# Kernel tuning notes

Hardware: AMD Instinct MI355X
Metric: run time of the kernel (lower is better)

Reference implementation:

```python
import jax, jax.numpy as jnp
import numpy as np

N = 50000
E = 1600000
NFEAT = 128
NHID = 128
NEG_SLOPE_ATT = 0.2   # GATConv attention leaky_relu
NEG_SLOPE_ACT = 0.01  # F.leaky_relu default between layers


def setup_inputs() -> dict:
    key = jax.random.key(0)
    ks = jax.random.split(key, 12)
    x = jax.random.normal(ks[0], (N, NFEAT), dtype=jnp.float32)
    edge_index = jax.random.randint(ks[1], (2, E), 0, N, dtype=jnp.int64)
    s1 = 1.0 / np.sqrt(NFEAT)
    s2 = 1.0 / np.sqrt(NHID)
    return {
        "x": x,
        "edge_index": edge_index,
        "W1": jax.random.normal(ks[2], (NFEAT, NHID), dtype=jnp.float32) * s1,
        "att_src1": jax.random.normal(ks[3], (NHID,), dtype=jnp.float32) * s2,
        "att_dst1": jax.random.normal(ks[4], (NHID,), dtype=jnp.float32) * s2,
        "b1": jnp.zeros((NHID,), dtype=jnp.float32),
        "W2": jax.random.normal(ks[5], (NHID, NHID), dtype=jnp.float32) * s2,
        "att_src2": jax.random.normal(ks[6], (NHID,), dtype=jnp.float32) * s2,
        "att_dst2": jax.random.normal(ks[7], (NHID,), dtype=jnp.float32) * s2,
        "b2": jnp.zeros((NHID,), dtype=jnp.float32),
    }


def _gat_conv(x, src, dst, W, a_src, a_dst, b):
    # single-head GATConv (PyG defaults), self-loops already in src/dst
    h = x @ W                                  # [N, nhid]
    alpha_s = h @ a_src                        # [N]
    alpha_d = h @ a_dst                        # [N]
    e = jax.nn.leaky_relu(alpha_s[src] + alpha_d[dst], NEG_SLOPE_ATT)  # [E']
    # softmax over incoming edges per destination node
    m = jax.ops.segment_max(e, dst, num_segments=N)
    e = jnp.exp(e - m[dst])
    denom = jax.ops.segment_sum(e, dst, num_segments=N)
    alpha = e / (denom[dst] + 1e-16)
    out = jax.ops.segment_sum(h[src] * alpha[:, None], dst, num_segments=N)
    return out + b


def reference(x, edge_index, W1, att_src1, att_dst1, b1, W2, att_src2, att_dst2, b2):
    loops = jnp.arange(N, dtype=edge_index.dtype)
    src = jnp.concatenate([edge_index[0], loops])  # add_self_loops=True
    dst = jnp.concatenate([edge_index[1], loops])
    h = _gat_conv(x, src, dst, W1, att_src1, att_dst1, b1)
    h = jax.nn.leaky_relu(h, NEG_SLOPE_ACT)
    out = _gat_conv(h, src, dst, W2, att_src2, att_dst2, b2)
    return out
```

## Files before the change

### kernel.cpp

```cpp
#include <hip/hip_runtime.h>
#include <hip/hip_fp16.h>

constexpr int N  = 50000;
constexpr int E  = 1600000;
constexpr int ET = E + N;
constexpr int NF = 128;
constexpr int BSH = 128;
constexpr int NB = (N + BSH - 1) / BSH;
constexpr int CAP = 8192;
constexpr int EPB  = 8192;
constexpr int NBLK = (ET + EPB - 1) / EPB;
constexpr int PACKW_BLKS = (2 * NF * NF + 1023) / 1024;
constexpr int GEMM1_BLKS = (N + 127) / 128;
constexpr int SCAPW = 128;

typedef _Float16 half8 __attribute__((ext_vector_type(8)));
typedef float    f32x4 __attribute__((ext_vector_type(4)));

__global__ __launch_bounds__(1024) void k_scatter_packw(
    const int* __restrict__ ei, int* __restrict__ bcur, int* __restrict__ packed,
    const float* __restrict__ W1, const float* __restrict__ W2,
    __half* __restrict__ P1, __half* __restrict__ P2) {
    int t = threadIdx.x;
    if (blockIdx.x >= NBLK) {
        int tid = (blockIdx.x - NBLK) * 1024 + t;
        if (tid >= 2 * NF * NF) return;
        int which = tid >> 14;
        int id = tid & (NF * NF - 1);
        int k = id >> 7, n = id & 127;
        const float* W = which ? W2 : W1;
        __half* P = which ? P2 : P1;
        int ks = k >> 5, r = k & 31, ct = n >> 4;
        int lane = ((r >> 3) << 4) | (n & 15);
        int j = r & 7;
        P[((ks * 8 + ct) * 64 + lane) * 8 + j] = __float2half_rn(W[k * NF + n]);
        return;
    }
    __shared__ int h[NB], lcur[NB], garr[NB];
    for (int i = t; i < NB; i += 1024) h[i] = 0;
    __syncthreads();
    int base = blockIdx.x * EPB;
    int pk[EPB / 1024];
    int bk[EPB / 1024];
#pragma unroll
    for (int k = 0; k < EPB / 1024; ++k) {
        int i = base + k * 1024 + t;
        if (i < ET) {
            int s, d;
            if (i < E) { s = ei[i]; d = ei[E + i]; } else { s = i - E; d = i - E; }
            bk[k] = d >> 7;
            pk[k] = s | ((d & (BSH - 1)) << 16);
            atomicAdd(&h[bk[k]], 1);
        } else bk[k] = -1;
    }
    __syncthreads();
    for (int i = t; i < NB; i += 1024) {
        lcur[i] = 0;
        garr[i] = i * CAP + (h[i] ? atomicAdd(&bcur[i], h[i]) : 0);
    }
    __syncthreads();
#pragma unroll
    for (int k = 0; k < EPB / 1024; ++k) {
        if (bk[k] >= 0) {
            int p = garr[bk[k]] + atomicAdd(&lcur[bk[k]], 1);
            packed[p] = pk[k];
        }
    }
}

template <typename AT>
__device__ __forceinline__ void gemm_rows16(
    const AT* __restrict__ A, const half8* __restrict__ BP,
    const float* __restrict__ asv, const float* __restrict__ adv,
    __half* __restrict__ H16, float* __restrict__ AS, float* __restrict__ AD,
    int base, int lane) {
    int row_a = base + (lane & 15);
    if (row_a >= N) row_a = N - 1;
    const AT* Arow = A + (size_t)row_a * NF;

    f32x4 acc[8] = {};
#pragma unroll
    for (int ks = 0; ks < 4; ++ks) {
        int eo = (ks * 4 + (lane >> 4)) * 8;
        half8 a;
        if constexpr (sizeof(AT) == 4) {
            float4 u = *(const float4*)(Arow + eo);
            float4 v = *(const float4*)(Arow + eo + 4);
            a[0] = (_Float16)u.x; a[1] = (_Float16)u.y; a[2] = (_Float16)u.z; a[3] = (_Float16)u.w;
            a[4] = (_Float16)v.x; a[5] = (_Float16)v.y; a[6] = (_Float16)v.z; a[7] = (_Float16)v.w;
        } else {
            a = ((const half8*)Arow)[ks * 4 + (lane >> 4)];
        }
#pragma unroll
        for (int ct = 0; ct < 8; ++ct) {
            half8 b = BP[(ks * 8 + ct) * 64 + lane];
            acc[ct] = __builtin_amdgcn_mfma_f32_16x16x32_f16(a, b, acc[ct], 0, 0, 0);
        }
    }

    int colb = lane & 15;
    int rowq = base + (lane >> 4) * 4;
    float ps[4] = {0.f, 0.f, 0.f, 0.f};
    float pd[4] = {0.f, 0.f, 0.f, 0.f};
#pragma unroll
    for (int ct = 0; ct < 8; ++ct) {
        int col = ct * 16 + colb;
        float av = asv[col], dv = adv[col];
#pragma unroll
        for (int r = 0; r < 4; ++r) {
            float hv = acc[ct][r];
            if (rowq + r < N) H16[(size_t)(rowq + r) * NF + col] = __float2half_rn(hv);
            ps[r] = fmaf(hv, av, ps[r]);
            pd[r] = fmaf(hv, dv, pd[r]);
        }
    }
#pragma unroll
    for (int r = 0; r < 4; ++r) {
#pragma unroll
        for (int o = 1; o <= 8; o <<= 1) {
            ps[r] += __shfl_xor(ps[r], o);
            pd[r] += __shfl_xor(pd[r], o);
        }
    }
    if (colb == 0) {
#pragma unroll
        for (int r = 0; r < 4; ++r) {
            if (rowq + r < N) { AS[rowq + r] = ps[r]; AD[rowq + r] = pd[r]; }
        }
    }
}

__global__ __launch_bounds__(512) void k_csr_gemm1(
    const int* __restrict__ packed, const int* __restrict__ bcur,
    int* __restrict__ offB, int* __restrict__ offE, unsigned short* __restrict__ srcs,
    const float* __restrict__ X, const __half* __restrict__ Wpk,
    const float* __restrict__ asv, const float* __restrict__ adv,
    __half* __restrict__ H16, float* __restrict__ AS, float* __restrict__ AD) {
    int t = threadIdx.x;
    if ((blockIdx.x & 1) == 0) {
        int blk = blockIdx.x >> 1;
        int wave = t >> 6, lane = t & 63;
        int base = blk * 128 + wave * 16;
        gemm_rows16<float>(X, (const half8*)Wpk, asv, adv, H16, AS, AD, base, lane);
        return;
    }
    int b = blockIdx.x >> 1;
    int s0 = b * CAP;
    int n = bcur[b];
    __shared__ int buf[CAP];
    __shared__ int h[BSH], bas[BSH], lcur[BSH];
    for (int i = t; i < n; i += 512) buf[i] = packed[s0 + i];
    if (t < BSH) { h[t] = 0; lcur[t] = 0; }
    __syncthreads();
    for (int i = t; i < n; i += 512)
        atomicAdd(&h[(buf[i] >> 16) & (BSH - 1)], 1);
    __syncthreads();
    if (t < 64) {
        int v0 = h[2 * t], v1 = h[2 * t + 1];
        int pair = v0 + v1, x = pair;
#pragma unroll
        for (int o = 1; o < 64; o <<= 1) {
            int y = __shfl_up(x, o);
            if (t >= o) x += y;
        }
        int e0 = s0 + x - pair;
        int e1 = e0 + v0;
        bas[2 * t] = e0; bas[2 * t + 1] = e1;
        int d = b * BSH + 2 * t;
        if (d < N)     { offB[d] = e0;     offE[d] = e1; }
        if (d + 1 < N) { offB[d + 1] = e1; offE[d + 1] = s0 + x; }
    }
    __syncthreads();
    for (int i = t; i < n; i += 512) {
        int p = buf[i];
        int dl = (p >> 16) & (BSH - 1);
        int pos = bas[dl] + atomicAdd(&lcur[dl], 1);
        srcs[pos] = (unsigned short)(p & 0xFFFF);
    }
}

__global__ __launch_bounds__(256) void k_gemm_mfma2(
    const __half* __restrict__ A, const __half* __restrict__ Wpk,
    const float* __restrict__ asv, const float* __restrict__ adv,
    __half* __restrict__ H16, float* __restrict__ AS, float* __restrict__ AD) {
    int t = threadIdx.x;
    int wave = t >> 6, lane = t & 63;
    int base = blockIdx.x * 64 + wave * 16;
    gemm_rows16<__half>(A, (const half8*)Wpk, asv, adv, H16, AS, AD, base, lane);
}

template <typename OUTT, int ACT>
__global__ __launch_bounds__(256) void k_aggregate(
    const __half* __restrict__ H16, const float* __restrict__ AS, const float* __restrict__ AD,
    const int* __restrict__ offB, const int* __restrict__ offE,
    const unsigned short* __restrict__ srcs,
    const float* __restrict__ bias, OUTT* __restrict__ OUT) {
    int wave = threadIdx.x >> 6, lane = threadIdx.x & 63;
    int d = blockIdx.x * 4 + wave;

    __shared__ float ssv[4][SCAPW];
    __shared__ unsigned short ssrc[4][SCAPW];

    int beg = offB[d], deg = offE[d] - beg;
    float ad = AD[d];

    float ls = 0.f;
    for (int i = lane; i < deg; i += 64) {
        int s = srcs[beg + i];
        float sv = AS[s] + ad;
        sv = (sv > 0.f) ? sv : 0.2f * sv;
        float e = __expf(fminf(sv, 60.f));
        if (i < SCAPW) { ssv[wave][i] = e; ssrc[wave][i] = (unsigned short)s; }
        ls += e;
    }
#pragma unroll
    for (int o = 1; o <= 32; o <<= 1) ls += __shfl_xor(ls, o);
    float inv = 1.f / (ls + 1e-16f);

    int tx = lane & 15, u = lane >> 4;
    float acc[8] = {0.f, 0.f, 0.f, 0.f, 0.f, 0.f, 0.f, 0.f};
    for (int j0 = 0; j0 < deg; j0 += 8) {
        int i0 = j0 + u, i1 = j0 + 4 + u;
        float e0 = 0.f, e1 = 0.f;
        int s0 = 0, s1 = 0;
        bool v0 = i0 < deg, v1 = i1 < deg;
        if (v0) {
            if (i0 < SCAPW) { e0 = ssv[wave][i0]; s0 = ssrc[wave][i0]; }
            else {
                s0 = srcs[beg + i0];
                float sv = AS[s0] + ad;
                sv = (sv > 0.f) ? sv : 0.2f * sv;
                e0 = __expf(fminf(sv, 60.f));
            }
        }
        if (v1) {
            if (i1 < SCAPW) { e1 = ssv[wave][i1]; s1 = ssrc[wave][i1]; }
            else {
                s1 = srcs[beg + i1];
                float sv = AS[s1] + ad;
                sv = (sv > 0.f) ? sv : 0.2f * sv;
                e1 = __expf(fminf(sv, 60.f));
            }
        }
        union { float4 f; __half2 h[4]; } va, vb;
        if (v0) va.f = *reinterpret_cast<const float4*>(H16 + (size_t)s0 * NF + tx * 8);
        if (v1) vb.f = *reinterpret_cast<const float4*>(H16 + (size_t)s1 * NF + tx * 8);
        if (v0) {
            float2 f0 = __half22float2(va.h[0]);
            float2 f1 = __half22float2(va.h[1]);
            float2 f2 = __half22float2(va.h[2]);
            float2 f3 = __half22float2(va.h[3]);
            acc[0] = fmaf(e0, f0.x, acc[0]); acc[1] = fmaf(e0, f0.y, acc[1]);
            acc[2] = fmaf(e0, f1.x, acc[2]); acc[3] = fmaf(e0, f1.y, acc[3]);
            acc[4] = fmaf(e0, f2.x, acc[4]); acc[5] = fmaf(e0, f2.y, acc[5]);
            acc[6] = fmaf(e0, f3.x, acc[6]); acc[7] = fmaf(e0, f3.y, acc[7]);
        }
        if (v1) {
            float2 f0 = __half22float2(vb.h[0]);
            float2 f1 = __half22float2(vb.h[1]);
            float2 f2 = __half22float2(vb.h[2]);
            float2 f3 = __half22float2(vb.h[3]);
            acc[0] = fmaf(e1, f0.x, acc[0]); acc[1] = fmaf(e1, f0.y, acc[1]);
            acc[2] = fmaf(e1, f1.x, acc[2]); acc[3] = fmaf(e1, f1.y, acc[3]);
            acc[4] = fmaf(e1, f2.x, acc[4]); acc[5] = fmaf(e1, f2.y, acc[5]);
            acc[6] = fmaf(e1, f3.x, acc[6]); acc[7] = fmaf(e1, f3.y, acc[7]);
        }
    }
#pragma unroll
    for (int o = 16; o <= 32; o <<= 1) {
#pragma unroll
        for (int i = 0; i < 8; ++i) acc[i] += __shfl_xor(acc[i], o);
    }
    if (lane < 16) {
        float o8[8];
#pragma unroll
        for (int i = 0; i < 8; ++i) {
            float v = acc[i] * inv + bias[tx * 8 + i];
            o8[i] = (ACT && v < 0.f) ? 0.01f * v : v;
        }
        if constexpr (sizeof(OUTT) == 2) {
            union { __half2 h[4]; float4 f; } pk;
            pk.h[0] = __floats2half2_rn(o8[0], o8[1]);
            pk.h[1] = __floats2half2_rn(o8[2], o8[3]);
            pk.h[2] = __floats2half2_rn(o8[4], o8[5]);
            pk.h[3] = __floats2half2_rn(o8[6], o8[7]);
            ((float4*)OUT)[(size_t)d * 16 + tx] = pk.f;
        } else {
            float4 w0 = {o8[0], o8[1], o8[2], o8[3]};
            float4 w1 = {o8[4], o8[5], o8[6], o8[7]};
            ((float4*)OUT)[(size_t)d * 32 + tx * 2]     = w0;
            ((float4*)OUT)[(size_t)d * 32 + tx * 2 + 1] = w1;
        }
    }
}

extern "C" void kernel_launch(void* const* d_in, const int* in_sizes, int n_in,
                              void* d_out, int out_size, void* d_ws, size_t ws_size,
                              hipStream_t stream) {
    const float* x   = (const float*)d_in[0];
    const int*   ei  = (const int*)d_in[1];
    const float* W1  = (const float*)d_in[2];
    const float* as1 = (const float*)d_in[3];
    const float* ad1 = (const float*)d_in[4];
    const float* b1  = (const float*)d_in[5];
    const float* W2  = (const float*)d_in[6];
    const float* as2 = (const float*)d_in[7];
    const float* ad2 = (const float*)d_in[8];
    const float* b2  = (const float*)d_in[9];
    float* out = (float*)d_out;

    char* p = (char*)d_ws;
    auto alloc = [&](size_t bytes) { char* r = p; p += (bytes + 255) & ~size_t(255); return (void*)r; };
    int* bcur  = (int*)alloc(sizeof(int) * NB);
    int* offB  = (int*)alloc(sizeof(int) * N);
    int* offE  = (int*)alloc(sizeof(int) * N);
    unsigned short* srcs = (unsigned short*)alloc(sizeof(unsigned short) * (size_t)NB * CAP);
    __half* H16   = (__half*)alloc(sizeof(__half) * (size_t)N * NF);
    __half* HMID16= (__half*)alloc(sizeof(__half) * (size_t)N * NF);
    __half* Wpk1  = (__half*)alloc(sizeof(__half) * NF * NF);
    __half* Wpk2  = (__half*)alloc(sizeof(__half) * NF * NF);
    float* AS  = (float*)alloc(sizeof(float) * N);
    float* AD  = (float*)alloc(sizeof(float) * N);
    int* packed = (int*)alloc(sizeof(int) * (size_t)NB * CAP);

    hipMemsetAsync(bcur, 0, sizeof(int) * NB, stream);
    k_scatter_packw<<<NBLK + PACKW_BLKS, 1024, 0, stream>>>(ei, bcur, packed, W1, W2, Wpk1, Wpk2);
    k_csr_gemm1<<<2 * GEMM1_BLKS, 512, 0, stream>>>(packed, bcur, offB, offE, srcs,
                                                    x, Wpk1, as1, ad1, H16, AS, AD);
    k_aggregate<__half, 1><<<N / 4, 256, 0, stream>>>(H16, AS, AD, offB, offE, srcs, b1, HMID16);
    k_gemm_mfma2<<<(N + 63) / 64, 256, 0, stream>>>(HMID16, Wpk2, as2, ad2, H16, AS, AD);
    k_aggregate<float, 0><<<N / 4, 256, 0, stream>>>(H16, AS, AD, offB, offE, srcs, b2, out);
}
```

Baseline: 178.2 us.

## Fuse layer-1 aggregation with layer-2 GEMM and precompute W2·att vectors

Merges the first aggregation kernel with the second-layer GEMM. Each 1024-thread block aggregates 16 destination rows, stages the activated fp16 rows in shared memory, and multiplies them by packed W2 with MFMA. The layer-2 attention scalars are computed directly from the fp32 activations using the precomputed vectors W2·att_src and W2·att_dst, built by an extra block in the scatter kernel. This removes the HMID round trip through global memory and one kernel launch. In exchange it uses larger blocks with a __syncthreads, which may lower occupancy and tie 16 rows of uneven degree to one barrier.

```diff
diff --git a/kernel.cpp b/kernel.cpp
--- a/kernel.cpp
+++ b/kernel.cpp
@@ -20,8 +20,22 @@
 __global__ __launch_bounds__(1024) void k_scatter_packw(
     const int* __restrict__ ei, int* __restrict__ bcur, int* __restrict__ packed,
     const float* __restrict__ W1, const float* __restrict__ W2,
-    __half* __restrict__ P1, __half* __restrict__ P2) {
+    __half* __restrict__ P1, __half* __restrict__ P2,
+    const float* __restrict__ as2, const float* __restrict__ ad2,
+    float* __restrict__ w2as, float* __restrict__ w2ad) {
     int t = threadIdx.x;
+    if (blockIdx.x == NBLK + PACKW_BLKS) {
+        if (t < NF) {
+            float ps = 0.f, pd = 0.f;
+            for (int j = 0; j < NF; ++j) {
+                float w = W2[t * NF + j];
+                ps = fmaf(w, as2[j], ps);
+                pd = fmaf(w, ad2[j], pd);
+            }
+            w2as[t] = ps; w2ad[t] = pd;
+        }
+        return;
+    }
     if (blockIdx.x >= NBLK) {
         int tid = (blockIdx.x - NBLK) * 1024 + t;
         if (tid >= 2 * NF * NF) return;
@@ -179,27 +193,19 @@
     }
 }
 
-__global__ __launch_bounds__(256) void k_gemm_mfma2(
-    const __half* __restrict__ A, const __half* __restrict__ Wpk,
-    const float* __restrict__ asv, const float* __restrict__ adv,
-    __half* __restrict__ H16, float* __restrict__ AS, float* __restrict__ AD) {
-    int t = threadIdx.x;
-    int wave = t >> 6, lane = t & 63;
-    int base = blockIdx.x * 64 + wave * 16;
-    gemm_rows16<__half>(A, (const half8*)Wpk, asv, adv, H16, AS, AD, base, lane);
-}
-
-template <typename OUTT, int ACT>
-__global__ __launch_bounds__(256) void k_aggregate(
-    const __half* __restrict__ H16, const float* __restrict__ AS, const float* __restrict__ AD,
+__global__ __launch_bounds__(1024) void k_agg1_gemm2(
+    const __half* __restrict__ H16in, const float* __restrict__ AS, const float* __restrict__ AD,
     const int* __restrict__ offB, const int* __restrict__ offE,
     const unsigned short* __restrict__ srcs,
-    const float* __restrict__ bias, OUTT* __restrict__ OUT) {
+    const float* __restrict__ b1, const __half* __restrict__ Wpk2,
+    const float* __restrict__ w2as, const float* __restrict__ w2ad,
+    __half* __restrict__ H16out, float* __restrict__ AS2, float* __restrict__ AD2) {
     int wave = threadIdx.x >> 6, lane = threadIdx.x & 63;
-    int d = blockIdx.x * 4 + wave;
-
-    __shared__ float ssv[4][SCAPW];
-    __shared__ unsigned short ssrc[4][SCAPW];
+    int d = blockIdx.x * 16 + wave;
+
+    __shared__ float ssv[16][SCAPW];
+    __shared__ unsigned short ssrc[16][SCAPW];
+    __shared__ __half Y[16][136];
 
     int beg = offB[d], deg = offE[d] - beg;
     float ad = AD[d];
@@ -243,6 +249,125 @@
             }
         }
         union { float4 f; __half2 h[4]; } va, vb;
+        if (v0) va.f = *reinterpret_cast<const float4*>(H16in + (size_t)s0 * NF + tx * 8);
+        if (v1) vb.f = *reinterpret_cast<const float4*>(H16in + (size_t)s1 * NF + tx * 8);
+        if (v0) {
+            float2 f0 = __half22float2(va.h[0]);
+            float2 f1 = __half22float2(va.h[1]);
+            float2 f2 = __half22float2(va.h[2]);
+            float2 f3 = __half22float2(va.h[3]);
+            acc[0] = fmaf(e0, f0.x, acc[0]); acc[1] = fmaf(e0, f0.y, acc[1]);
+            acc[2] = fmaf(e0, f1.x, acc[2]); acc[3] = fmaf(e0, f1.y, acc[3]);
+            acc[4] = fmaf(e0, f2.x, acc[4]); acc[5] = fmaf(e0, f2.y, acc[5]);
+            acc[6] = fmaf(e0, f3.x, acc[6]); acc[7] = fmaf(e0, f3.y, acc[7]);
+        }
+        if (v1) {
+            float2 f0 = __half22float2(vb.h[0]);
+            float2 f1 = __half22float2(vb.h[1]);
+            float2 f2 = __half22float2(vb.h[2]);
+            float2 f3 = __half22float2(vb.h[3]);
+            acc[0] = fmaf(e1, f0.x, acc[0]); acc[1] = fmaf(e1, f0.y, acc[1]);
+            acc[2] = fmaf(e1, f1.x, acc[2]); acc[3] = fmaf(e1, f1.y, acc[3]);
+            acc[4] = fmaf(e1, f2.x, acc[4]); acc[5] = fmaf(e1, f2.y, acc[5]);
+            acc[6] = fmaf(e1, f3.x, acc[6]); acc[7] = fmaf(e1, f3.y, acc[7]);
+        }
+    }
+#pragma unroll
+    for (int o = 16; o <= 32; o <<= 1) {
+#pragma unroll
+        for (int i = 0; i < 8; ++i) acc[i] += __shfl_xor(acc[i], o);
+    }
+    float y[8];
+    float ps = 0.f, pd = 0.f;
+#pragma unroll
+    for (int i = 0; i < 8; ++i) {
+        float v = acc[i] * inv + b1[tx * 8 + i];
+        v = (v < 0.f) ? 0.01f * v : v;
+        y[i] = v;
+        ps = fmaf(v, w2as[tx * 8 + i], ps);
+        pd = fmaf(v, w2ad[tx * 8 + i], pd);
+    }
+#pragma unroll
+    for (int o = 1; o <= 8; o <<= 1) { ps += __shfl_xor(ps, o); pd += __shfl_xor(pd, o); }
+    if (lane == 0) { AS2[d] = ps; AD2[d] = pd; }
+    if (lane < 16) {
+        half8 hv;
+#pragma unroll
+        for (int i = 0; i < 8; ++i) hv[i] = (_Float16)y[i];
+        *(half8*)(&Y[wave][tx * 8]) = hv;
+    }
+    __syncthreads();
+    if (wave < 8) {
+        const half8* BP = (const half8*)Wpk2;
+        f32x4 c4 = {};
+#pragma unroll
+        for (int ks = 0; ks < 4; ++ks) {
+            half8 a = *(const half8*)(&Y[lane & 15][ks * 32 + (lane >> 4) * 8]);
+            half8 b = BP[(ks * 8 + wave) * 64 + lane];
+            c4 = __builtin_amdgcn_mfma_f32_16x16x32_f16(a, b, c4, 0, 0, 0);
+        }
+        int base = blockIdx.x * 16;
+        int colb = lane & 15;
+        int rowq = (lane >> 4) * 4;
+#pragma unroll
+        for (int r = 0; r < 4; ++r)
+            H16out[(size_t)(base + rowq + r) * NF + wave * 16 + colb] = __float2half_rn(c4[r]);
+    }
+}
+
+__global__ __launch_bounds__(256) void k_aggregate2(
+    const __half* __restrict__ H16, const float* __restrict__ AS, const float* __restrict__ AD,
+    const int* __restrict__ offB, const int* __restrict__ offE,
+    const unsigned short* __restrict__ srcs,
+    const float* __restrict__ bias, float* __restrict__ OUT) {
+    int wave = threadIdx.x >> 6, lane = threadIdx.x & 63;
+    int d = blockIdx.x * 4 + wave;
+
+    __shared__ float ssv[4][SCAPW];
+    __shared__ unsigned short ssrc[4][SCAPW];
+
+    int beg = offB[d], deg = offE[d] - beg;
+    float ad = AD[d];
+
+    float ls = 0.f;
+    for (int i = lane; i < deg; i += 64) {
+        int s = srcs[beg + i];
+        float sv = AS[s] + ad;
+        sv = (sv > 0.f) ? sv : 0.2f * sv;
+        float e = __expf(fminf(sv, 60.f));
+        if (i < SCAPW) { ssv[wave][i] = e; ssrc[wave][i] = (unsigned short)s; }
+        ls += e;
+    }
+#pragma unroll
+    for (int o = 1; o <= 32; o <<= 1) ls += __shfl_xor(ls, o);
+    float inv = 1.f / (ls + 1e-16f);
+
+    int tx = lane & 15, u = lane >> 4;
+    float acc[8] = {0.f, 0.f, 0.f, 0.f, 0.f, 0.f, 0.f, 0.f};
+    for (int j0 = 0; j0 < deg; j0 += 8) {
+        int i0 = j0 + u, i1 = j0 + 4 + u;
+        float e0 = 0.f, e1 = 0.f;
+        int s0 = 0, s1 = 0;
+        bool v0 = i0 < deg, v1 = i1 < deg;
+        if (v0) {
+            if (i0 < SCAPW) { e0 = ssv[wave][i0]; s0 = ssrc[wave][i0]; }
+            else {
+                s0 = srcs[beg + i0];
+                float sv = AS[s0] + ad;
+                sv = (sv > 0.f) ? sv : 0.2f * sv;
+                e0 = __expf(fminf(sv, 60.f));
+            }
+        }
+        if (v1) {
+            if (i1 < SCAPW) { e1 = ssv[wave][i1]; s1 = ssrc[wave][i1]; }
+            else {
+                s1 = srcs[beg + i1];
+                float sv = AS[s1] + ad;
+                sv = (sv > 0.f) ? sv : 0.2f * sv;
+                e1 = __expf(fminf(sv, 60.f));
+            }
+        }
+        union { float4 f; __half2 h[4]; } va, vb;
         if (v0) va.f = *reinterpret_cast<const float4*>(H16 + (size_t)s0 * NF + tx * 8);
         if (v1) vb.f = *reinterpret_cast<const float4*>(H16 + (size_t)s1 * NF + tx * 8);
         if (v0) {
@@ -272,25 +397,14 @@
         for (int i = 0; i < 8; ++i) acc[i] += __shfl_xor(acc[i], o);
     }
     if (lane < 16) {
+        float4 w0, w1;
         float o8[8];
 #pragma unroll
-        for (int i = 0; i < 8; ++i) {
-            float v = acc[i] * inv + bias[tx * 8 + i];
-            o8[i] = (ACT && v < 0.f) ? 0.01f * v : v;
-        }
-        if constexpr (sizeof(OUTT) == 2) {
-            union { __half2 h[4]; float4 f; } pk;
-            pk.h[0] = __floats2half2_rn(o8[0], o8[1]);
-            pk.h[1] = __floats2half2_rn(o8[2], o8[3]);
-            pk.h[2] = __floats2half2_rn(o8[4], o8[5]);
-            pk.h[3] = __floats2half2_rn(o8[6], o8[7]);
-            ((float4*)OUT)[(size_t)d * 16 + tx] = pk.f;
-        } else {
-            float4 w0 = {o8[0], o8[1], o8[2], o8[3]};
-            float4 w1 = {o8[4], o8[5], o8[6], o8[7]};
-            ((float4*)OUT)[(size_t)d * 32 + tx * 2]     = w0;
-            ((float4*)OUT)[(size_t)d * 32 + tx * 2 + 1] = w1;
-        }
+        for (int i = 0; i < 8; ++i) o8[i] = acc[i] * inv + bias[tx * 8 + i];
+        w0 = {o8[0], o8[1], o8[2], o8[3]};
+        w1 = {o8[4], o8[5], o8[6], o8[7]};
+        ((float4*)OUT)[(size_t)d * 32 + tx * 2]     = w0;
+        ((float4*)OUT)[(size_t)d * 32 + tx * 2 + 1] = w1;
     }
 }
 
@@ -315,19 +429,24 @@
     int* offB  = (int*)alloc(sizeof(int) * N);
     int* offE  = (int*)alloc(sizeof(int) * N);
     unsigned short* srcs = (unsigned short*)alloc(sizeof(unsigned short) * (size_t)NB * CAP);
-    __half* H16   = (__half*)alloc(sizeof(__half) * (size_t)N * NF);
-    __half* HMID16= (__half*)alloc(sizeof(__half) * (size_t)N * NF);
+    __half* H16a  = (__half*)alloc(sizeof(__half) * (size_t)N * NF);
+    __half* H16b  = (__half*)alloc(sizeof(__half) * (size_t)N * NF);
     __half* Wpk1  = (__half*)alloc(sizeof(__half) * NF * NF);
     __half* Wpk2  = (__half*)alloc(sizeof(__half) * NF * NF);
-    float* AS  = (float*)alloc(sizeof(float) * N);
-    float* AD  = (float*)alloc(sizeof(float) * N);
+    float* AS1 = (float*)alloc(sizeof(float) * N);
+    float* AD1 = (float*)alloc(sizeof(float) * N);
+    float* AS2 = (float*)alloc(sizeof(float) * N);
+    float* AD2 = (float*)alloc(sizeof(float) * N);
+    float* w2as = (float*)alloc(sizeof(float) * NF);
+    float* w2ad = (float*)alloc(sizeof(float) * NF);
     int* packed = (int*)alloc(sizeof(int) * (size_t)NB * CAP);
 
     hipMemsetAsync(bcur, 0, sizeof(int) * NB, stream);
-    k_scatter_packw<<<NBLK + PACKW_BLKS, 1024, 0, stream>>>(ei, bcur, packed, W1, W2, Wpk1, Wpk2);
+    k_scatter_packw<<<NBLK + PACKW_BLKS + 1, 1024, 0, stream>>>(
+        ei, bcur, packed, W1, W2, Wpk1, Wpk2, as2, ad2, w2as, w2ad);
     k_csr_gemm1<<<2 * GEMM1_BLKS, 512, 0, stream>>>(packed, bcur, offB, offE, srcs,
-                                                    x, Wpk1, as1, ad1, H16, AS, AD);
-    k_aggregate<__half, 1><<<N / 4, 256, 0, stream>>>(H16, AS, AD, offB, offE, srcs, b1, HMID16);
-    k_gemm_mfma2<<<(N + 63) / 64, 256, 0, stream>>>(HMID16, Wpk2, as2, ad2, H16, AS, AD);
-    k_aggregate<float, 0><<<N / 4, 256, 0, stream>>>(H16, AS, AD, offB, offE, srcs, b2, out);
-}
+                                                    x, Wpk1, as1, ad1, H16a, AS1, AD1);
+    k_agg1_gemm2<<<N / 16, 1024, 0, stream>>>(H16a, AS1, AD1, offB, offE, srcs,
+                                              b1, Wpk2, w2as, w2ad, H16b, AS2, AD2);
+    k_aggregate2<<<N / 4, 256, 0, stream>>>(H16b, AS2, AD2, offB, offE, srcs, b2, out);
+}
```

Result: faster. 173.4 us (-2.7%).
